# Kernel optimization log

Hardware: AMD Instinct MI355X
Metric: run time of the kernel (lower is better)

## Reference

```python
import jax, jax.numpy as jnp
import numpy as np

NEG_SLOPE = 0.2
EPS = 1e-16
HEADS1, OUT1 = 4, 32
HEADS2, OUT2 = 1, 32


def _gat_conv(x, W, a_src, a_dst, bias, src, dst, num_nodes, heads, out_c, concat):
    # x: [N, F_in], W: [F_in, heads*out_c], a_*: [heads, out_c]
    h = (x @ W).reshape(num_nodes, heads, out_c)            # [N, H, C]
    alpha_src = (h * a_src).sum(-1)                          # [N, H]
    alpha_dst = (h * a_dst).sum(-1)                          # [N, H]
    e = jax.nn.leaky_relu(alpha_src[src] + alpha_dst[dst], NEG_SLOPE)  # [E, H]
    # softmax over incoming edges of each destination node (PyG softmax)
    m = jax.ops.segment_max(e, dst, num_segments=num_nodes)
    ex = jnp.exp(e - m[dst])
    s = jax.ops.segment_sum(ex, dst, num_segments=num_nodes)
    alpha = ex / (s[dst] + EPS)                              # [E, H]
    out = jax.ops.segment_sum(h[src] * alpha[:, :, None], dst,
                              num_segments=num_nodes)        # [N, H, C]
    out = out.reshape(num_nodes, heads * out_c) if concat else out.mean(axis=1)
    return out + bias


def setup_inputs() -> dict:
    key = jax.random.key(0)
    ks = jax.random.split(key, 10)
    N, E, F_IN = 50000, 1600000, 128
    sc = 0.1
    return {
        "x": jax.random.normal(ks[0], (N, F_IN), jnp.float32),
        "edge_index": jax.random.randint(ks[1], (2, E), 0, N, jnp.int32),
        "W1": jax.random.normal(ks[2], (F_IN, HEADS1 * OUT1), jnp.float32) * sc,
        "a_src1": jax.random.normal(ks[3], (HEADS1, OUT1), jnp.float32) * sc,
        "a_dst1": jax.random.normal(ks[4], (HEADS1, OUT1), jnp.float32) * sc,
        "b1": jax.random.normal(ks[5], (HEADS1 * OUT1,), jnp.float32) * sc,
        "W2": jax.random.normal(ks[6], (HEADS1 * OUT1, HEADS2 * OUT2), jnp.float32) * sc,
        "a_src2": jax.random.normal(ks[7], (HEADS2, OUT2), jnp.float32) * sc,
        "a_dst2": jax.random.normal(ks[8], (HEADS2, OUT2), jnp.float32) * sc,
        "b2": jax.random.normal(ks[9], (OUT2,), jnp.float32) * sc,
    }


def reference(x, edge_index, W1, a_src1, a_dst1, b1, W2, a_src2, a_dst2, b2):
    N = x.shape[0]
    # PyG GATConv default add_self_loops=True
    loops = jnp.arange(N, dtype=edge_index.dtype)
    src = jnp.concatenate([edge_index[0], loops])
    dst = jnp.concatenate([edge_index[1], loops])
    h = _gat_conv(x, W1, a_src1, a_dst1, b1, src, dst, N, HEADS1, OUT1, True)
    h = jax.nn.elu(h)
    return _gat_conv(h, W2, a_src2, a_dst2, b2, src, dst, N, HEADS2, OUT2, False)
```

## Files before the change

kernel.cpp:

```cpp
#include <hip/hip_runtime.h>
#include <math.h>

#define NEG_SLOPE 0.2f
#define EPSV 1e-16f
#define NPART 8

typedef _Float16 half4 __attribute__((ext_vector_type(4)));
typedef _Float16 half8 __attribute__((ext_vector_type(8)));
typedef float floatx2 __attribute__((ext_vector_type(2)));


__global__ void k_scan_blk(const int* __restrict__ degp, int N,
                           int* __restrict__ rowptr, int* __restrict__ bsum){
    int b = blockIdx.x, t = threadIdx.x;
    int base = b * 1024 + t * 4;
    int v[4];
    #pragma unroll
    for (int j = 0; j < 4; j++){
        int n = base + j, s = 0;
        if (n < N){
            #pragma unroll
            for (int p = 0; p < NPART; p++) s += degp[p * N + n];
        }
        v[j] = s;
    }
    int s = v[0] + v[1] + v[2] + v[3];
    int lane = t & 63, wid = t >> 6;
    int x = s;
    #pragma unroll
    for (int off = 1; off < 64; off <<= 1){
        int y = __shfl_up(x, off, 64);
        if (lane >= off) x += y;
    }
    __shared__ int ws[4];
    if (lane == 63) ws[wid] = x;
    __syncthreads();
    int woff = 0;
    for (int w = 0; w < wid; w++) woff += ws[w];
    int run = woff + x - s;
    #pragma unroll
    for (int j = 0; j < 4; j++){
        if (base + j < N) rowptr[base + j] = run;
        run += v[j];
    }
    if (t == 255) bsum[b] = woff + x;
}

__global__ void k_finalize(const int* __restrict__ bsum, const int* __restrict__ degp,
                           int N, int ET,
                           int* __restrict__ rowptr, int* __restrict__ poff){
    int b = blockIdx.x, t = threadIdx.x;
    int n = b * 256 + t;
    int chunk = (b * 256) >> 10;
    int off = 0;
    for (int c = 0; c < chunk; c++) off += bsum[c];
    if (n < N){
        int r = rowptr[n] + off;
        rowptr[n] = r;
        int run = r;
        #pragma unroll
        for (int p = 0; p < NPART; p++){
            poff[p * N + n] = run;
            run += degp[p * N + n];
        }
    }
    if (n == 0) rowptr[N] = ET;
}

__launch_bounds__(256)
__global__ void k_scatter2(const int* __restrict__ ei, int E, int ET, int N,
                           const int* __restrict__ poff,
                           const unsigned short* __restrict__ rank,
                           int* __restrict__ csr_src){
    int i = blockIdx.x * 256 + threadIdx.x;
    if (i >= ET) return;
    int s, d;
    if (i < E){ s = ei[i]; d = ei[E + i]; } else { s = i - E; d = s; }
    int pr = rank[i];
    int p = pr >> 13, r = pr & 0x1FFF;
    csr_src[poff[p * N + d] + r] = s;
}


__launch_bounds__(256, 5)
__global__ void k_gemm1_hist(const float* __restrict__ x, const float* __restrict__ W1,
                             const float* __restrict__ a_src, const float* __restrict__ a_dst,
                             _Float16* __restrict__ h1h, float* __restrict__ asrc1,
                             float* __restrict__ adst1, int N, int nGemmBlk,
                             const int* __restrict__ ei, int E, int ET,
                             unsigned int* __restrict__ degp, unsigned short* __restrict__ rank){
    __shared__ float xl[64 * 128];
    int t = threadIdx.x;
    if ((int)blockIdx.x >= nGemmBlk){
        int p = __builtin_amdgcn_s_getreg((3 << 11) | 20) & 7;
        int base = (blockIdx.x - nGemmBlk) * 1024 + t;
        #pragma unroll
        for (int j = 0; j < 4; j++){
            int i = base + j * 256;
            if (i < ET){
                int d = (i < E) ? ei[E + i] : (i - E);
                unsigned r = __hip_atomic_fetch_add(&degp[(size_t)p * N + d], 1u,
                                 __ATOMIC_RELAXED, __HIP_MEMORY_SCOPE_WORKGROUP);
                rank[i] = (unsigned short)((p << 13) | r);
            }
        }
        return;
    }
    int cg = t & 31, rs = t >> 5;
    int n0 = blockIdx.x * 64;
    for (int idx = t; idx < 2048; idx += 256){
        int row = idx >> 5, k4 = idx & 31;
        float4 v = {0.f, 0.f, 0.f, 0.f};
        if (n0 + row < N) v = *(const float4*)&x[(size_t)(n0 + row) * 128 + k4 * 4];
        *(float4*)&xl[row * 128 + k4 * 4] = v;
    }
    __syncthreads();
    float4 acc[8];
    #pragma unroll
    for (int j = 0; j < 8; j++) acc[j] = (float4){0.f, 0.f, 0.f, 0.f};
    for (int hc = 0; hc < 16; hc++){
        float4 wr[8];
        #pragma unroll
        for (int k = 0; k < 8; k++)
            wr[k] = *(const float4*)&W1[(hc * 8 + k) * 128 + cg * 4];
        #pragma unroll
        for (int kb = 0; kb < 8; kb += 4){
            float4 xv[8];
            #pragma unroll
            for (int j = 0; j < 8; j++)
                xv[j] = *(const float4*)&xl[(rs + 8 * j) * 128 + hc * 8 + kb];
            #pragma unroll
            for (int kk = 0; kk < 4; kk++){
                float4 w = wr[kb + kk];
                #pragma unroll
                for (int j = 0; j < 8; j++){
                    float xs = ((const float*)&xv[j])[kk];
                    acc[j].x = fmaf(xs, w.x, acc[j].x);
                    acc[j].y = fmaf(xs, w.y, acc[j].y);
                    acc[j].z = fmaf(xs, w.z, acc[j].z);
                    acc[j].w = fmaf(xs, w.w, acc[j].w);
                }
            }
        }
    }
    float4 a4s = *(const float4*)&a_src[cg * 4];
    float4 a4d = *(const float4*)&a_dst[cg * 4];
    #pragma unroll
    for (int j = 0; j < 8; j++){
        int n = n0 + rs + 8 * j;
        if (n >= N) continue;
        float4 a = acc[j];
        half4 hv;
        hv.x = (_Float16)a.x; hv.y = (_Float16)a.y;
        hv.z = (_Float16)a.z; hv.w = (_Float16)a.w;
        *(half4*)&h1h[((size_t)n << 7) + (cg << 2)] = hv;
        float vs = a.x * a4s.x + a.y * a4s.y + a.z * a4s.z + a.w * a4s.w;
        float vd = a.x * a4d.x + a.y * a4d.y + a.z * a4d.z + a.w * a4d.w;
        #pragma unroll
        for (int m = 1; m <= 4; m <<= 1){
            vs += __shfl_xor(vs, m, 64);
            vd += __shfl_xor(vd, m, 64);
        }
        if ((cg & 7) == 0){
            int head = cg >> 3;
            asrc1[n * 4 + head] = vs;
            adst1[n * 4 + head] = vd;
        }
    }
}


__launch_bounds__(256)
__global__ void k_agg1(const int* __restrict__ rowptr, const int* __restrict__ csr_src,
                       const float* __restrict__ asrc1, const float* __restrict__ adst1,
                       const _Float16* __restrict__ h1h,
                       const float* __restrict__ b1, float* __restrict__ x2){
    int t = threadIdx.x;
    int n = blockIdx.x * 4 + (t >> 6);
    int lane = t & 63, g = lane >> 4, l = lane & 15, head = l >> 2;
    int start = rowptr[n], end = rowptr[n + 1];
    float adn = adst1[(n << 2) + head];
    const char* hb = (const char*)h1h;
    const char* ab = (const char*)asrc1;
    int hoff = l << 4;
    int aoff = head << 2;
    floatx2 r0[4], r1[4], r2[4], r3[4];
    #pragma unroll
    for (int j = 0; j < 4; j++){
        r0[j] = (floatx2)0.f; r1[j] = (floatx2)0.f;
        r2[j] = (floatx2)0.f; r3[j] = (floatx2)0.f;
    }
    float s0a = 0.f, s1a = 0.f, s2a = 0.f, s3a = 0.f;
    int i = start + g;
    for (; i + 12 < end; i += 16){
        int sa = csr_src[i];
        int sb = csr_src[i + 4];
        int sc = csr_src[i + 8];
        int sd = csr_src[i + 12];
        float ea = *(const float*)(ab + (sa << 4) + aoff) + adn;
        float eb = *(const float*)(ab + (sb << 4) + aoff) + adn;
        float ec = *(const float*)(ab + (sc << 4) + aoff) + adn;
        float ed = *(const float*)(ab + (sd << 4) + aoff) + adn;
        ea = fmaxf(ea, NEG_SLOPE * ea);
        eb = fmaxf(eb, NEG_SLOPE * eb);
        ec = fmaxf(ec, NEG_SLOPE * ec);
        ed = fmaxf(ed, NEG_SLOPE * ed);
        float wa = __expf(ea);
        float wb = __expf(eb);
        float wc = __expf(ec);
        float wd = __expf(ed);
        half8 ha = *(const half8*)(hb + (sa << 8) + hoff);
        half8 hbv = *(const half8*)(hb + (sb << 8) + hoff);
        half8 hcv = *(const half8*)(hb + (sc << 8) + hoff);
        half8 hdv = *(const half8*)(hb + (sd << 8) + hoff);
        s0a += wa; s1a += wb; s2a += wc; s3a += wd;
        floatx2 wa2 = {wa, wa}, wb2 = {wb, wb}, wc2 = {wc, wc}, wd2 = {wd, wd};
        #pragma unroll
        for (int j = 0; j < 4; j++){
            floatx2 ca = {(float)ha[2*j], (float)ha[2*j+1]};
            floatx2 cb = {(float)hbv[2*j], (float)hbv[2*j+1]};
            floatx2 cc = {(float)hcv[2*j], (float)hcv[2*j+1]};
            floatx2 cd = {(float)hdv[2*j], (float)hdv[2*j+1]};
            r0[j] = wa2 * ca + r0[j];
            r1[j] = wb2 * cb + r1[j];
            r2[j] = wc2 * cc + r2[j];
            r3[j] = wd2 * cd + r3[j];
        }
    }
    for (; i < end; i += 4){
        int sa = csr_src[i];
        float ea = *(const float*)(ab + (sa << 4) + aoff) + adn;
        ea = fmaxf(ea, NEG_SLOPE * ea);
        float wa = __expf(ea);
        half8 ha = *(const half8*)(hb + (sa << 8) + hoff);
        s0a += wa;
        floatx2 wa2 = {wa, wa};
        #pragma unroll
        for (int j = 0; j < 4; j++){
            floatx2 ca = {(float)ha[2*j], (float)ha[2*j+1]};
            r0[j] = wa2 * ca + r0[j];
        }
    }
    float r[9];
    #pragma unroll
    for (int j = 0; j < 4; j++){
        floatx2 c = (r0[j] + r1[j]) + (r2[j] + r3[j]);
        r[2*j] = c.x; r[2*j+1] = c.y;
    }
    r[8] = (s0a + s1a) + (s2a + s3a);
    #pragma unroll
    for (int m = 16; m <= 32; m <<= 1)
        #pragma unroll
        for (int j = 0; j < 9; j++) r[j] += __shfl_xor(r[j], m, 64);
    if (g == 0){
        float inv = 1.f / (r[8] + EPSV);
        float o[8];
        #pragma unroll
        for (int j = 0; j < 8; j++){
            float v = r[j] * inv + b1[l * 8 + j];
            o[j] = (v > 0.f) ? v : expm1f(v);
        }
        float4 o0 = {o[0], o[1], o[2], o[3]};
        float4 o1 = {o[4], o[5], o[6], o[7]};
        *(float4*)&x2[((size_t)n << 7) + (l << 3)]     = o0;
        *(float4*)&x2[((size_t)n << 7) + (l << 3) + 4] = o1;
    }
}


__launch_bounds__(256)
__global__ void k_gemm2(const float* __restrict__ x2, const float* __restrict__ W2,
                        const float* __restrict__ a_src, const float* __restrict__ a_dst,
                        _Float16* __restrict__ h2h, float* __restrict__ asrc2,
                        float* __restrict__ adst2, int N){
    __shared__ float Wl[128 * 32];
    __shared__ float xl[64 * 128];
    int t = threadIdx.x;
    int cg = t & 7, ns = t >> 3;
    for (int idx = t; idx < 1024; idx += 256)
        *(float4*)&Wl[idx * 4] = *(const float4*)&W2[idx * 4];
    int n0 = blockIdx.x * 64;
    for (int idx = t; idx < 2048; idx += 256){
        int row = idx >> 5, k4 = idx & 31;
        float4 v = {0.f, 0.f, 0.f, 0.f};
        if (n0 + row < N) v = *(const float4*)&x2[(size_t)(n0 + row) * 128 + k4 * 4];
        *(float4*)&xl[row * 128 + k4 * 4] = v;
    }
    __syncthreads();
    float4 acc0 = {0,0,0,0}, acc1 = {0,0,0,0};
    #pragma unroll 2
    for (int k = 0; k < 128; k += 4){
        float4 xv0 = *(float4*)&xl[(ns      ) * 128 + k];
        float4 xv1 = *(float4*)&xl[(ns + 32) * 128 + k];
        #pragma unroll
        for (int kk = 0; kk < 4; kk++){
            float4 w = *(float4*)&Wl[(k + kk) * 32 + cg * 4];
            float x0 = ((float*)&xv0)[kk];
            float x1 = ((float*)&xv1)[kk];
            acc0.x = fmaf(x0, w.x, acc0.x); acc0.y = fmaf(x0, w.y, acc0.y);
            acc0.z = fmaf(x0, w.z, acc0.z); acc0.w = fmaf(x0, w.w, acc0.w);
            acc1.x = fmaf(x1, w.x, acc1.x); acc1.y = fmaf(x1, w.y, acc1.y);
            acc1.z = fmaf(x1, w.z, acc1.z); acc1.w = fmaf(x1, w.w, acc1.w);
        }
    }
    float4 a4s = *(const float4*)&a_src[cg * 4];
    float4 a4d = *(const float4*)&a_dst[cg * 4];
    float4 accs[2] = {acc0, acc1};
    #pragma unroll
    for (int j = 0; j < 2; j++){
        int n = n0 + ns + 32 * j;
        if (n >= N) continue;
        float4 a = accs[j];
        half4 hv;
        hv.x = (_Float16)a.x; hv.y = (_Float16)a.y;
        hv.z = (_Float16)a.z; hv.w = (_Float16)a.w;
        *(half4*)&h2h[((size_t)n << 5) + (cg << 2)] = hv;
        float vs = a.x * a4s.x + a.y * a4s.y + a.z * a4s.z + a.w * a4s.w;
        float vd = a.x * a4d.x + a.y * a4d.y + a.z * a4d.z + a.w * a4d.w;
        #pragma unroll
        for (int m = 1; m <= 4; m <<= 1){
            vs += __shfl_xor(vs, m, 64);
            vd += __shfl_xor(vd, m, 64);
        }
        if (cg == 0){ asrc2[n] = vs; adst2[n] = vd; }
    }
}


__launch_bounds__(256)
__global__ void k_agg2(const int* __restrict__ rowptr, const int* __restrict__ csr_src,
                       const float* __restrict__ asrc2, const float* __restrict__ adst2,
                       const _Float16* __restrict__ h2h,
                       const float* __restrict__ b2, float* __restrict__ out){
    int t = threadIdx.x;
    int n = blockIdx.x * 8 + (t >> 5);
    int l5 = t & 31, g = l5 >> 3, l = l5 & 7;
    int start = rowptr[n], end = rowptr[n + 1];
    float adn = adst2[n];
    const char* hb = (const char*)h2h;
    const char* ab = (const char*)asrc2;
    int hoff = l << 3;
    floatx2 a0[2], a1[2], a2[2], a3[2];
    a0[0] = (floatx2)0.f; a0[1] = (floatx2)0.f;
    a1[0] = (floatx2)0.f; a1[1] = (floatx2)0.f;
    a2[0] = (floatx2)0.f; a2[1] = (floatx2)0.f;
    a3[0] = (floatx2)0.f; a3[1] = (floatx2)0.f;
    float s0a = 0.f, s1a = 0.f, s2a = 0.f, s3a = 0.f;
    int i = start + g;
    for (; i + 12 < end; i += 16){
        int sa = csr_src[i];
        int sb = csr_src[i + 4];
        int sc = csr_src[i + 8];
        int sd = csr_src[i + 12];
        float ea = *(const float*)(ab + (sa << 2)) + adn;
        float eb = *(const float*)(ab + (sb << 2)) + adn;
        float ec = *(const float*)(ab + (sc << 2)) + adn;
        float ed = *(const float*)(ab + (sd << 2)) + adn;
        ea = fmaxf(ea, NEG_SLOPE * ea);
        eb = fmaxf(eb, NEG_SLOPE * eb);
        ec = fmaxf(ec, NEG_SLOPE * ec);
        ed = fmaxf(ed, NEG_SLOPE * ed);
        float wa = __expf(ea);
        float wb = __expf(eb);
        float wc = __expf(ec);
        float wd = __expf(ed);
        half4 ha = *(const half4*)(hb + (sa << 6) + hoff);
        half4 hbv = *(const half4*)(hb + (sb << 6) + hoff);
        half4 hcv = *(const half4*)(hb + (sc << 6) + hoff);
        half4 hdv = *(const half4*)(hb + (sd << 6) + hoff);
        s0a += wa; s1a += wb; s2a += wc; s3a += wd;
        floatx2 wa2 = {wa, wa}, wb2 = {wb, wb}, wc2 = {wc, wc}, wd2 = {wd, wd};
        floatx2 ca0 = {(float)ha.x, (float)ha.y},  ca1 = {(float)ha.z, (float)ha.w};
        floatx2 cb0 = {(float)hbv.x, (float)hbv.y}, cb1 = {(float)hbv.z, (float)hbv.w};
        floatx2 cc0 = {(float)hcv.x, (float)hcv.y}, cc1 = {(float)hcv.z, (float)hcv.w};
        floatx2 cd0 = {(float)hdv.x, (float)hdv.y}, cd1 = {(float)hdv.z, (float)hdv.w};
        a0[0] = wa2 * ca0 + a0[0]; a0[1] = wa2 * ca1 + a0[1];
        a1[0] = wb2 * cb0 + a1[0]; a1[1] = wb2 * cb1 + a1[1];
        a2[0] = wc2 * cc0 + a2[0]; a2[1] = wc2 * cc1 + a2[1];
        a3[0] = wd2 * cd0 + a3[0]; a3[1] = wd2 * cd1 + a3[1];
    }
    for (; i < end; i += 4){
        int sa = csr_src[i];
        float ea = *(const float*)(ab + (sa << 2)) + adn;
        ea = fmaxf(ea, NEG_SLOPE * ea);
        float wa = __expf(ea);
        half4 ha = *(const half4*)(hb + (sa << 6) + hoff);
        s0a += wa;
        floatx2 wa2 = {wa, wa};
        floatx2 ca0 = {(float)ha.x, (float)ha.y}, ca1 = {(float)ha.z, (float)ha.w};
        a0[0] = wa2 * ca0 + a0[0]; a0[1] = wa2 * ca1 + a0[1];
    }
    floatx2 m0 = (a0[0] + a1[0]) + (a2[0] + a3[0]);
    floatx2 m1 = (a0[1] + a1[1]) + (a2[1] + a3[1]);
    float4 acc = {m0.x, m0.y, m1.x, m1.y};
    float ssum = (s0a + s1a) + (s2a + s3a);
    #pragma unroll
    for (int m = 8; m <= 16; m <<= 1){
        acc.x += __shfl_xor(acc.x, m, 64);
        acc.y += __shfl_xor(acc.y, m, 64);
        acc.z += __shfl_xor(acc.z, m, 64);
        acc.w += __shfl_xor(acc.w, m, 64);
        ssum  += __shfl_xor(ssum,  m, 64);
    }
    if (g == 0){
        float inv = 1.f / (ssum + EPSV);
        const float4 b4 = *(const float4*)&b2[l * 4];
        float4 o;
        o.x = acc.x * inv + b4.x; o.y = acc.y * inv + b4.y;
        o.z = acc.z * inv + b4.z; o.w = acc.w * inv + b4.w;
        *(float4*)&out[((size_t)n << 5) + l * 4] = o;
    }
}


extern "C" void kernel_launch(void* const* d_in, const int* in_sizes, int n_in,
                              void* d_out, int out_size, void* d_ws, size_t ws_size,
                              hipStream_t stream){
    const float* x      = (const float*)d_in[0];
    const int*   ei     = (const int*)  d_in[1];
    const float* W1     = (const float*)d_in[2];
    const float* a_src1 = (const float*)d_in[3];
    const float* a_dst1 = (const float*)d_in[4];
    const float* b1     = (const float*)d_in[5];
    const float* W2     = (const float*)d_in[6];
    const float* a_src2 = (const float*)d_in[7];
    const float* a_dst2 = (const float*)d_in[8];
    const float* b2     = (const float*)d_in[9];
    float* out = (float*)d_out;

    int N  = in_sizes[0] / 128;
    int E  = in_sizes[1] / 2;
    int ET = E + N;
    int nScanBlk = (N + 1023) / 1024;
    int G  = (ET + 255) / 256;
    int GH = (ET + 1023) / 1024;
    int nGemmBlk = (N + 63) / 64;

    char* ws = (char*)d_ws;
    size_t off = 0;
    auto alloc = [&](size_t bytes) -> char* {
        char* p = ws + off;
        off += (bytes + 255) & ~(size_t)255;
        return p;
    };
    int*            degp    = (int*)           alloc((size_t)NPART * N * 4);
    int*            rowptr  = (int*)           alloc((size_t)(N + 1) * 4);
    int*            bsum    = (int*)           alloc((size_t)nScanBlk * 4);
    unsigned short* rank    = (unsigned short*)alloc((size_t)ET * 2);
    int*            poff    = (int*)           alloc((size_t)NPART * N * 4);
    int*            csr_src = (int*)           alloc((size_t)ET * 4);
    _Float16*       h1h     = (_Float16*)      alloc((size_t)N * 128 * 2);
    float*          x2      = (float*)         alloc((size_t)N * 128 * 4);
    float*          asrc1   = (float*)         alloc((size_t)N * 4 * 4);
    float*          adst1   = (float*)         alloc((size_t)N * 4 * 4);
    _Float16*       h2h     = (_Float16*)      alloc((size_t)N * 32 * 2);
    float*          asrc2   = (float*)         alloc((size_t)N * 4);
    float*          adst2   = (float*)         alloc((size_t)N * 4);

    hipMemsetAsync(degp, 0, (size_t)NPART * N * 4, stream);
    hipLaunchKernelGGL(k_gemm1_hist, dim3(nGemmBlk + GH), dim3(256), 0, stream,
                       x, W1, a_src1, a_dst1, h1h, asrc1, adst1, N, nGemmBlk,
                       ei, E, ET, (unsigned int*)degp, rank);
    hipLaunchKernelGGL(k_scan_blk,  dim3(nScanBlk), dim3(256), 0, stream, degp, N, rowptr, bsum);
    hipLaunchKernelGGL(k_finalize,  dim3((N + 255) / 256), dim3(256), 0, stream, bsum, degp, N, ET, rowptr, poff);
    hipLaunchKernelGGL(k_scatter2,  dim3(G), dim3(256), 0, stream, ei, E, ET, N, poff, rank, csr_src);
    hipLaunchKernelGGL(k_agg1,      dim3(N / 4), dim3(256), 0, stream, rowptr, csr_src, asrc1, adst1, h1h, b1, x2);
    hipLaunchKernelGGL(k_gemm2,     dim3((N + 63) / 64), dim3(256), 0, stream, x2, W2, a_src2, a_dst2, h2h, asrc2, adst2, N);
    hipLaunchKernelGGL(k_agg2,      dim3(N / 8), dim3(256), 0, stream, rowptr, csr_src, asrc2, adst2, h2h, b2, out);
}
```

Measured before the change: 319.9 us.

## Assign one node per lane group in aggregation kernels instead of splitting edges

Both aggregation kernels now give each lane group (16 lanes in layer 1, 8 lanes in layer 2) its own destination node rather than splitting one node's edges across four groups. This removes the cross-group shuffle reduction and packs four times as many nodes into each block. The cost is more divergence in loop trip count within a wavefront, since degrees vary per node, and each group walks its full edge list serially. A bounds check is added so the grid no longer needs N to be divisible by the per-block node count.

```diff
diff --git a/kernel.cpp b/kernel.cpp
--- a/kernel.cpp
+++ b/kernel.cpp
@@ -174,12 +174,15 @@
 __global__ void k_agg1(const int* __restrict__ rowptr, const int* __restrict__ csr_src,
                        const float* __restrict__ asrc1, const float* __restrict__ adst1,
                        const _Float16* __restrict__ h1h,
-                       const float* __restrict__ b1, float* __restrict__ x2){
+                       const float* __restrict__ b1, float* __restrict__ x2, int N){
     int t = threadIdx.x;
-    int n = blockIdx.x * 4 + (t >> 6);
-    int lane = t & 63, g = lane >> 4, l = lane & 15, head = l >> 2;
-    int start = rowptr[n], end = rowptr[n + 1];
-    float adn = adst1[(n << 2) + head];
+    int lane = t & 63;
+    int g = lane >> 4, l = lane & 15, head = l >> 2;
+    int n = blockIdx.x * 16 + ((t >> 6) << 2) + g;
+    bool valid = (n < N);
+    int nn = valid ? n : 0;
+    int start = rowptr[nn], end = rowptr[nn + 1];
+    float adn = adst1[(nn << 2) + head];
     const char* hb = (const char*)h1h;
     const char* ab = (const char*)asrc1;
     int hoff = l << 4;
@@ -191,12 +194,12 @@
         r2[j] = (floatx2)0.f; r3[j] = (floatx2)0.f;
     }
     float s0a = 0.f, s1a = 0.f, s2a = 0.f, s3a = 0.f;
-    int i = start + g;
-    for (; i + 12 < end; i += 16){
+    int i = start;
+    for (; i + 3 < end; i += 4){
         int sa = csr_src[i];
-        int sb = csr_src[i + 4];
-        int sc = csr_src[i + 8];
-        int sd = csr_src[i + 12];
+        int sb = csr_src[i + 1];
+        int sc = csr_src[i + 2];
+        int sd = csr_src[i + 3];
         float ea = *(const float*)(ab + (sa << 4) + aoff) + adn;
         float eb = *(const float*)(ab + (sb << 4) + aoff) + adn;
         float ec = *(const float*)(ab + (sc << 4) + aoff) + adn;
@@ -227,7 +230,7 @@
             r3[j] = wd2 * cd + r3[j];
         }
     }
-    for (; i < end; i += 4){
+    for (; i < end; i++){
         int sa = csr_src[i];
         float ea = *(const float*)(ab + (sa << 4) + aoff) + adn;
         ea = fmaxf(ea, NEG_SLOPE * ea);
@@ -241,24 +244,17 @@
             r0[j] = wa2 * ca + r0[j];
         }
     }
-    float r[9];
-    #pragma unroll
-    for (int j = 0; j < 4; j++){
-        floatx2 c = (r0[j] + r1[j]) + (r2[j] + r3[j]);
-        r[2*j] = c.x; r[2*j+1] = c.y;
-    }
-    r[8] = (s0a + s1a) + (s2a + s3a);
-    #pragma unroll
-    for (int m = 16; m <= 32; m <<= 1)
-        #pragma unroll
-        for (int j = 0; j < 9; j++) r[j] += __shfl_xor(r[j], m, 64);
-    if (g == 0){
-        float inv = 1.f / (r[8] + EPSV);
+    if (valid){
+        float ssum = (s0a + s1a) + (s2a + s3a);
+        float inv = 1.f / (ssum + EPSV);
         float o[8];
         #pragma unroll
-        for (int j = 0; j < 8; j++){
-            float v = r[j] * inv + b1[l * 8 + j];
-            o[j] = (v > 0.f) ? v : expm1f(v);
+        for (int j = 0; j < 4; j++){
+            floatx2 c = (r0[j] + r1[j]) + (r2[j] + r3[j]);
+            float v0 = c.x * inv + b1[l * 8 + 2*j];
+            float v1 = c.y * inv + b1[l * 8 + 2*j + 1];
+            o[2*j]   = (v0 > 0.f) ? v0 : expm1f(v0);
+            o[2*j+1] = (v1 > 0.f) ? v1 : expm1f(v1);
         }
         float4 o0 = {o[0], o[1], o[2], o[3]};
         float4 o1 = {o[4], o[5], o[6], o[7]};
@@ -331,12 +327,15 @@
 __global__ void k_agg2(const int* __restrict__ rowptr, const int* __restrict__ csr_src,
                        const float* __restrict__ asrc2, const float* __restrict__ adst2,
                        const _Float16* __restrict__ h2h,
-                       const float* __restrict__ b2, float* __restrict__ out){
+                       const float* __restrict__ b2, float* __restrict__ out, int N){
     int t = threadIdx.x;
-    int n = blockIdx.x * 8 + (t >> 5);
-    int l5 = t & 31, g = l5 >> 3, l = l5 & 7;
-    int start = rowptr[n], end = rowptr[n + 1];
-    float adn = adst2[n];
+    int lane = t & 63;
+    int g = lane >> 3, l = lane & 7;
+    int n = blockIdx.x * 32 + ((t >> 6) << 3) + g;
+    bool valid = (n < N);
+    int nn = valid ? n : 0;
+    int start = rowptr[nn], end = rowptr[nn + 1];
+    float adn = adst2[nn];
     const char* hb = (const char*)h2h;
     const char* ab = (const char*)asrc2;
     int hoff = l << 3;
@@ -346,12 +345,12 @@
     a2[0] = (floatx2)0.f; a2[1] = (floatx2)0.f;
     a3[0] = (floatx2)0.f; a3[1] = (floatx2)0.f;
     float s0a = 0.f, s1a = 0.f, s2a = 0.f, s3a = 0.f;
-    int i = start + g;
-    for (; i + 12 < end; i += 16){
+    int i = start;
+    for (; i + 3 < end; i += 4){
         int sa = csr_src[i];
-        int sb = csr_src[i + 4];
-        int sc = csr_src[i + 8];
-        int sd = csr_src[i + 12];
+        int sb = csr_src[i + 1];
+        int sc = csr_src[i + 2];
+        int sd = csr_src[i + 3];
         float ea = *(const float*)(ab + (sa << 2)) + adn;
         float eb = *(const float*)(ab + (sb << 2)) + adn;
         float ec = *(const float*)(ab + (sc << 2)) + adn;
@@ -379,7 +378,7 @@
         a2[0] = wc2 * cc0 + a2[0]; a2[1] = wc2 * cc1 + a2[1];
         a3[0] = wd2 * cd0 + a3[0]; a3[1] = wd2 * cd1 + a3[1];
     }
-    for (; i < end; i += 4){
+    for (; i < end; i++){
         int sa = csr_src[i];
         float ea = *(const float*)(ab + (sa << 2)) + adn;
         ea = fmaxf(ea, NEG_SLOPE * ea);
@@ -390,25 +389,16 @@
         floatx2 ca0 = {(float)ha.x, (float)ha.y}, ca1 = {(float)ha.z, (float)ha.w};
         a0[0] = wa2 * ca0 + a0[0]; a0[1] = wa2 * ca1 + a0[1];
     }
-    floatx2 m0 = (a0[0] + a1[0]) + (a2[0] + a3[0]);
-    floatx2 m1 = (a0[1] + a1[1]) + (a2[1] + a3[1]);
-    float4 acc = {m0.x, m0.y, m1.x, m1.y};
-    float ssum = (s0a + s1a) + (s2a + s3a);
-    #pragma unroll
-    for (int m = 8; m <= 16; m <<= 1){
-        acc.x += __shfl_xor(acc.x, m, 64);
-        acc.y += __shfl_xor(acc.y, m, 64);
-        acc.z += __shfl_xor(acc.z, m, 64);
-        acc.w += __shfl_xor(acc.w, m, 64);
-        ssum  += __shfl_xor(ssum,  m, 64);
-    }
-    if (g == 0){
+    if (valid){
+        floatx2 m0 = (a0[0] + a1[0]) + (a2[0] + a3[0]);
+        floatx2 m1 = (a0[1] + a1[1]) + (a2[1] + a3[1]);
+        float ssum = (s0a + s1a) + (s2a + s3a);
         float inv = 1.f / (ssum + EPSV);
         const float4 b4 = *(const float4*)&b2[l * 4];
         float4 o;
-        o.x = acc.x * inv + b4.x; o.y = acc.y * inv + b4.y;
-        o.z = acc.z * inv + b4.z; o.w = acc.w * inv + b4.w;
-        *(float4*)&out[((size_t)n << 5) + l * 4] = o;
+        o.x = m0.x * inv + b4.x; o.y = m0.y * inv + b4.y;
+        o.z = m1.x * inv + b4.z; o.w = m1.y * inv + b4.w;
+        *(float4*)&out[((size_t)n << 5) + (l << 2)] = o;
     }
 }
 
@@ -464,7 +454,7 @@
     hipLaunchKernelGGL(k_scan_blk,  dim3(nScanBlk), dim3(256), 0, stream, degp, N, rowptr, bsum);
     hipLaunchKernelGGL(k_finalize,  dim3((N + 255) / 256), dim3(256), 0, stream, bsum, degp, N, ET, rowptr, poff);
     hipLaunchKernelGGL(k_scatter2,  dim3(G), dim3(256), 0, stream, ei, E, ET, N, poff, rank, csr_src);
-    hipLaunchKernelGGL(k_agg1,      dim3(N / 4), dim3(256), 0, stream, rowptr, csr_src, asrc1, adst1, h1h, b1, x2);
+    hipLaunchKernelGGL(k_agg1,      dim3((N + 15) / 16), dim3(256), 0, stream, rowptr, csr_src, asrc1, adst1, h1h, b1, x2, N);
     hipLaunchKernelGGL(k_gemm2,     dim3((N + 63) / 64), dim3(256), 0, stream, x2, W2, a_src2, a_dst2, h2h, asrc2, adst2, N);
-    hipLaunchKernelGGL(k_agg2,      dim3(N / 8), dim3(256), 0, stream, rowptr, csr_src, asrc2, adst2, h2h, b2, out);
-}
+    hipLaunchKernelGGL(k_agg2,      dim3((N + 31) / 32), dim3(256), 0, stream, rowptr, csr_src, asrc2, adst2, h2h, b2, out, N);
+}
```

New measurement: 301.9 us. -5.6%, faster.
